# Performance work log

Measured on AMD Instinct MI355X. Metric: run time of the kernel, lower is better.

Reference implementation:

```python
import jax, jax.numpy as jnp
import numpy as np
from jax import lax

SCALES = [4, 8, 16]
K_PER_SCALE = 4


def setup_inputs() -> dict:
    key = jax.random.key(0)
    B, N, D = 32, 4096, 384  # N = 64*64 perfect square
    features = jax.random.normal(key, (B, N, D), dtype=jnp.float32)
    return {"features": features}


def _kmeans_pp(feats, key, k):
    """k-means++ seeding on feats [N, D]; returns [k, D] centers.

    Faithful to torch version: first center uniform random, subsequent
    centers sampled with prob proportional to squared min distance
    (cdist is euclidean; probs = min_dist**2 == squared distance).
    Incremental min over squared distances is equivalent to recomputing
    cdist to all centers and taking the min each iteration.
    """
    N = feats.shape[0]
    k0, k1 = jax.random.split(key)
    idx0 = jax.random.randint(k0, (), 0, N)
    c0 = feats[idx0]  # [D]
    min_sq = jnp.sum((feats - c0) ** 2, axis=1)  # [N] squared dists

    def step(min_sq, kk):
        probs = min_sq / (min_sq.sum() + 1e-8)
        idx = jax.random.categorical(kk, jnp.log(probs + 1e-12))
        c = feats[idx]
        d = jnp.sum((feats - c) ** 2, axis=1)
        return jnp.minimum(min_sq, d), c

    keys = jax.random.split(k1, k - 1)
    _, rest = lax.scan(step, min_sq, keys)  # rest: [k-1, D]
    return jnp.concatenate([c0[None], rest], axis=0)


def reference(features):
    B, N, D = features.shape
    H = W = int(np.sqrt(N))
    x = features.reshape(B, H, W, D)
    base = jax.random.key(42)
    all_slots = []
    for si, s in enumerate(SCALES):
        # adaptive_avg_pool2d with H divisible by s == block mean
        pooled = x.reshape(B, s, H // s, s, W // s, D).mean(axis=(2, 4))  # [B,s,s,D]
        flat = pooled.reshape(B, s * s, D)
        bkeys = jax.random.split(jax.random.fold_in(base, si), B)
        cents = jax.vmap(lambda f, kk: _kmeans_pp(f, kk, K_PER_SCALE))(flat, bkeys)
        all_slots.append(cents)  # [B, k, D]
    return jnp.concatenate(all_slots, axis=1)  # [B, len(scales)*k, D]
```

## Files before the change

kernel.cpp:

```cpp
#include <hip/hip_runtime.h>
#include <stdint.h>

#define D_ 384
#define NPTS 4096
#define W4_OFF 0
#define W8_OFF 196608
#define W16_OFF 983040

__device__ __forceinline__ void tf_round(uint32_t& x0, uint32_t& x1, int r) {
  x0 += x1;
  x1 = (x1 << r) | (x1 >> (32 - r));
  x1 ^= x0;
}

__device__ void tf2x32(uint32_t k0, uint32_t k1, uint32_t x0, uint32_t x1,
                       uint32_t& y0, uint32_t& y1) {
  uint32_t ks2 = k0 ^ k1 ^ 0x1BD11BDAu;
  x0 += k0; x1 += k1;
  tf_round(x0, x1, 13); tf_round(x0, x1, 15); tf_round(x0, x1, 26); tf_round(x0, x1, 6);
  x0 += k1; x1 += ks2 + 1u;
  tf_round(x0, x1, 17); tf_round(x0, x1, 29); tf_round(x0, x1, 16); tf_round(x0, x1, 24);
  x0 += ks2; x1 += k0 + 2u;
  tf_round(x0, x1, 13); tf_round(x0, x1, 15); tf_round(x0, x1, 26); tf_round(x0, x1, 6);
  x0 += k0; x1 += k1 + 3u;
  tf_round(x0, x1, 17); tf_round(x0, x1, 29); tf_round(x0, x1, 16); tf_round(x0, x1, 24);
  x0 += k1; x1 += ks2 + 4u;
  tf_round(x0, x1, 13); tf_round(x0, x1, 15); tf_round(x0, x1, 26); tf_round(x0, x1, 6);
  x0 += ks2; x1 += k0 + 5u;
  y0 = x0; y1 = x1;
}

__global__ __launch_bounds__(256) void pool16_kernel(const float* __restrict__ feats,
                                                     float* __restrict__ ws) {
  int g = blockIdx.x * 256 + threadIdx.x;
  int q = g % 96;
  int cell = (g / 96) & 255;
  int b = g / (96 * 256);
  int ch = cell >> 4, cw = cell & 15;
  const float* fb = feats + (size_t)b * NPTS * D_;
  float ax = 0.f, ay = 0.f, az = 0.f, aw = 0.f;
  #pragma unroll
  for (int dh = 0; dh < 4; ++dh) {
    int h = ch * 4 + dh;
    #pragma unroll
    for (int dw = 0; dw < 4; ++dw) {
      int w = cw * 4 + dw;
      float4 v = *(const float4*)(fb + ((size_t)(h * 64 + w)) * D_ + q * 4);
      ax += v.x; ay += v.y; az += v.z; aw += v.w;
    }
  }
  float4 o = { ax * (1.f/16.f), ay * (1.f/16.f), az * (1.f/16.f), aw * (1.f/16.f) };
  *(float4*)(ws + W16_OFF + ((size_t)(b * 256 + cell)) * D_ + q * 4) = o;
}

__global__ __launch_bounds__(256) void pool8_kernel(float* __restrict__ ws) {
  int g = blockIdx.x * 256 + threadIdx.x;
  int q = g % 96;
  int c8 = (g / 96) & 63;
  int b = g / (96 * 64);
  int p = c8 >> 3, r = c8 & 7;
  float ax = 0.f, ay = 0.f, az = 0.f, aw = 0.f;
  #pragma unroll
  for (int a = 0; a < 2; ++a)
    #pragma unroll
    for (int c = 0; c < 2; ++c) {
      int cell = (p * 2 + a) * 16 + (r * 2 + c);
      float4 v = *(const float4*)(ws + W16_OFF + ((size_t)(b * 256 + cell)) * D_ + q * 4);
      ax += v.x; ay += v.y; az += v.z; aw += v.w;
    }
  float4 o = { ax * 0.25f, ay * 0.25f, az * 0.25f, aw * 0.25f };
  *(float4*)(ws + W8_OFF + ((size_t)(b * 64 + c8)) * D_ + q * 4) = o;
}

__global__ __launch_bounds__(256) void pool4_kernel(float* __restrict__ ws) {
  int g = blockIdx.x * 256 + threadIdx.x;
  int q = g % 96;
  int c4 = (g / 96) & 15;
  int b = g / (96 * 16);
  int p = c4 >> 2, r = c4 & 3;
  float ax = 0.f, ay = 0.f, az = 0.f, aw = 0.f;
  #pragma unroll
  for (int a = 0; a < 2; ++a)
    #pragma unroll
    for (int c = 0; c < 2; ++c) {
      int cell = (p * 2 + a) * 8 + (r * 2 + c);
      float4 v = *(const float4*)(ws + W8_OFF + ((size_t)(b * 64 + cell)) * D_ + q * 4);
      ax += v.x; ay += v.y; az += v.z; aw += v.w;
    }
  float4 o = { ax * 0.25f, ay * 0.25f, az * 0.25f, aw * 0.25f };
  *(float4*)(ws + W4_OFF + ((size_t)(b * 16 + c4)) * D_ + q * 4) = o;
}

__global__ __launch_bounds__(512) void kmeans_kernel(const float* __restrict__ ws,
                                                     float* __restrict__ out) {
  int blk = blockIdx.x;
  int si = blk / 32;
  int b  = blk % 32;
  int n  = (si == 0) ? 16 : (si == 1) ? 64 : 256;

  const float* pooled;
  if (si == 0)      pooled = ws + W4_OFF  + (size_t)b * 16  * D_;
  else if (si == 1) pooled = ws + W8_OFF  + (size_t)b * 64  * D_;
  else              pooled = ws + W16_OFF + (size_t)b * 256 * D_;
  float* ob = out + ((size_t)b * 12 + si * 4) * D_;

  __shared__ __align__(16) float4 csh4[96];
  __shared__ float minsq[256];
  __shared__ uint32_t skey[3][2];
  __shared__ int sidx;
  __shared__ float ssum;
  __shared__ float wred[4];
  __shared__ float wmaxv[4];
  __shared__ int   wmaxi[4];

  int tid  = threadIdx.x;
  int row  = tid >> 1;
  int part = tid & 1;
  int lane = tid & 63;
  int wv   = tid >> 6;

  if (tid == 0) {
    uint32_t f0, f1, bk0, bk1;
    tf2x32(0u, 42u, 0u, (uint32_t)si, f0, f1);
    tf2x32(f0, f1, 0u, (uint32_t)b, bk0, bk1);
    uint32_t k00, k01, k10, k11;
    tf2x32(bk0, bk1, 0u, 0u, k00, k01);
    tf2x32(bk0, bk1, 0u, 1u, k10, k11);
    uint32_t q0, q1, l0, l1;
    tf2x32(k00, k01, 0u, 1u, q0, q1);
    tf2x32(q0, q1, 0u, 0u, l0, l1);
    sidx = (int)((l0 ^ l1) & (uint32_t)(n - 1));
    for (int t = 0; t < 3; ++t) {
      uint32_t a, bb;
      tf2x32(k10, k11, 0u, (uint32_t)t, a, bb);
      skey[t][0] = a; skey[t][1] = bb;
    }
  }
  if (tid < 256) minsq[tid] = 0.f;

  float4 xr[48];
  if (row < n) {
    const float4* rp = (const float4*)(pooled + (size_t)row * D_ + part * 192);
    #pragma unroll
    for (int k = 0; k < 48; ++k) xr[k] = rp[k];
  }
  __syncthreads();

  if (row == sidx) {
    float4* cb = csh4 + part * 48;
    float4* op = (float4*)(ob + part * 192);
    #pragma unroll
    for (int k = 0; k < 48; ++k) { cb[k] = xr[k]; op[k] = xr[k]; }
  }
  __syncthreads();

  if (row < n) {
    float acc = 0.f;
    #pragma unroll
    for (int k = 0; k < 48; ++k) {
      float4 c4 = csh4[part * 48 + k];
      float dx = xr[k].x - c4.x, dy = xr[k].y - c4.y;
      float dz = xr[k].z - c4.z, dw = xr[k].w - c4.w;
      acc += dx * dx; acc += dy * dy; acc += dz * dz; acc += dw * dw;
    }
    acc += __shfl_xor(acc, 1);
    if (part == 0) minsq[row] = acc;
  }
  __syncthreads();

  const float TINY = __uint_as_float(0x00800000u);

  for (int t = 0; t < 3; ++t) {
    if (tid < 256) {
      float v = minsq[tid];
      #pragma unroll
      for (int m = 1; m < 64; m <<= 1) v += __shfl_xor(v, m);
      if (lane == 0) wred[wv] = v;
    }
    __syncthreads();
    if (tid == 0) ssum = ((wred[0] + wred[1]) + (wred[2] + wred[3])) + 1e-8f;
    __syncthreads();

    if (tid < 256) {
      float z = -1e30f;
      if (tid < n) {
        float prob  = minsq[tid] / ssum;
        float logit = logf(prob + 1e-12f);
        uint32_t y0, y1;
        tf2x32(skey[t][0], skey[t][1], 0u, (uint32_t)tid, y0, y1);
        uint32_t bits = y0 ^ y1;
        float f = __uint_as_float((bits >> 9) | 0x3F800000u) - 1.0f;
        float u = (f > 0.f) ? f : TINY;
        z = -logf(-logf(u)) + logit;
      }
      float bv = z; int bi = tid;
      #pragma unroll
      for (int m = 1; m < 64; m <<= 1) {
        float ov = __shfl_xor(bv, m);
        int   oi = __shfl_xor(bi, m);
        if (ov > bv || (ov == bv && oi < bi)) { bv = ov; bi = oi; }
      }
      if (lane == 0) { wmaxv[wv] = bv; wmaxi[wv] = bi; }
    }
    __syncthreads();
    if (tid == 0) {
      float cv = wmaxv[0]; int ci = wmaxi[0];
      for (int w2 = 1; w2 < 4; ++w2)
        if (wmaxv[w2] > cv || (wmaxv[w2] == cv && wmaxi[w2] < ci)) { cv = wmaxv[w2]; ci = wmaxi[w2]; }
      sidx = ci;
    }
    __syncthreads();

    if (row == sidx) {
      float4* cb = csh4 + part * 48;
      float4* op = (float4*)(ob + (size_t)(t + 1) * D_ + part * 192);
      #pragma unroll
      for (int k = 0; k < 48; ++k) { cb[k] = xr[k]; op[k] = xr[k]; }
    }
    __syncthreads();

    if (row < n) {
      float acc = 0.f;
      #pragma unroll
      for (int k = 0; k < 48; ++k) {
        float4 c4 = csh4[part * 48 + k];
        float dx = xr[k].x - c4.x, dy = xr[k].y - c4.y;
        float dz = xr[k].z - c4.z, dw = xr[k].w - c4.w;
        acc += dx * dx; acc += dy * dy; acc += dz * dz; acc += dw * dw;
      }
      acc += __shfl_xor(acc, 1);
      if (part == 0) minsq[row] = fminf(minsq[row], acc);
    }
    __syncthreads();
  }
}

extern "C" void kernel_launch(void* const* d_in, const int* in_sizes, int n_in,
                              void* d_out, int out_size, void* d_ws, size_t ws_size,
                              hipStream_t stream) {
  const float* feats = (const float*)d_in[0];
  float* out = (float*)d_out;
  float* ws  = (float*)d_ws;

  pool16_kernel<<<3072, 256, 0, stream>>>(feats, ws);
  pool8_kernel<<<768, 256, 0, stream>>>(ws);
  pool4_kernel<<<192, 256, 0, stream>>>(ws);
  kmeans_kernel<<<96, 512, 0, stream>>>(ws, out);
}
```

Baseline: 66.43 us.

## Fuse 8x8 and 4x4 pooling into the kmeans kernel from 16x16 pooled data

Drops the separate pool8 and pool4 kernels. The kmeans blocks now compute the coarser pooled rows directly from the 16x16 pooled workspace: the 8-scale rows are averaged in registers, and the 4-scale rows go through a shared-memory buffer. This removes two kernel launches and their workspace round trips. In exchange, the small-scale blocks do extra loads, use more shared memory, and partially unroll the register-load loops.

Result: slower. 127.7 us (+92.2%).

```diff
diff --git a/kernel.cpp b/kernel.cpp
--- a/kernel.cpp
+++ b/kernel.cpp
@@ -3,9 +3,6 @@
 
 #define D_ 384
 #define NPTS 4096
-#define W4_OFF 0
-#define W8_OFF 196608
-#define W16_OFF 983040
 
 __device__ __forceinline__ void tf_round(uint32_t& x0, uint32_t& x1, int r) {
   x0 += x1;
@@ -50,45 +47,7 @@
     }
   }
   float4 o = { ax * (1.f/16.f), ay * (1.f/16.f), az * (1.f/16.f), aw * (1.f/16.f) };
-  *(float4*)(ws + W16_OFF + ((size_t)(b * 256 + cell)) * D_ + q * 4) = o;
-}
-
-__global__ __launch_bounds__(256) void pool8_kernel(float* __restrict__ ws) {
-  int g = blockIdx.x * 256 + threadIdx.x;
-  int q = g % 96;
-  int c8 = (g / 96) & 63;
-  int b = g / (96 * 64);
-  int p = c8 >> 3, r = c8 & 7;
-  float ax = 0.f, ay = 0.f, az = 0.f, aw = 0.f;
-  #pragma unroll
-  for (int a = 0; a < 2; ++a)
-    #pragma unroll
-    for (int c = 0; c < 2; ++c) {
-      int cell = (p * 2 + a) * 16 + (r * 2 + c);
-      float4 v = *(const float4*)(ws + W16_OFF + ((size_t)(b * 256 + cell)) * D_ + q * 4);
-      ax += v.x; ay += v.y; az += v.z; aw += v.w;
-    }
-  float4 o = { ax * 0.25f, ay * 0.25f, az * 0.25f, aw * 0.25f };
-  *(float4*)(ws + W8_OFF + ((size_t)(b * 64 + c8)) * D_ + q * 4) = o;
-}
-
-__global__ __launch_bounds__(256) void pool4_kernel(float* __restrict__ ws) {
-  int g = blockIdx.x * 256 + threadIdx.x;
-  int q = g % 96;
-  int c4 = (g / 96) & 15;
-  int b = g / (96 * 16);
-  int p = c4 >> 2, r = c4 & 3;
-  float ax = 0.f, ay = 0.f, az = 0.f, aw = 0.f;
-  #pragma unroll
-  for (int a = 0; a < 2; ++a)
-    #pragma unroll
-    for (int c = 0; c < 2; ++c) {
-      int cell = (p * 2 + a) * 8 + (r * 2 + c);
-      float4 v = *(const float4*)(ws + W8_OFF + ((size_t)(b * 64 + cell)) * D_ + q * 4);
-      ax += v.x; ay += v.y; az += v.z; aw += v.w;
-    }
-  float4 o = { ax * 0.25f, ay * 0.25f, az * 0.25f, aw * 0.25f };
-  *(float4*)(ws + W4_OFF + ((size_t)(b * 16 + c4)) * D_ + q * 4) = o;
+  *(float4*)(ws + ((size_t)(b * 256 + cell)) * D_ + q * 4) = o;
 }
 
 __global__ __launch_bounds__(512) void kmeans_kernel(const float* __restrict__ ws,
@@ -98,12 +57,10 @@
   int b  = blk % 32;
   int n  = (si == 0) ? 16 : (si == 1) ? 64 : 256;
 
-  const float* pooled;
-  if (si == 0)      pooled = ws + W4_OFF  + (size_t)b * 16  * D_;
-  else if (si == 1) pooled = ws + W8_OFF  + (size_t)b * 64  * D_;
-  else              pooled = ws + W16_OFF + (size_t)b * 256 * D_;
+  const float4* w16b = (const float4*)(ws + (size_t)b * 256 * D_);
   float* ob = out + ((size_t)b * 12 + si * 4) * D_;
 
+  __shared__ __align__(16) float4 p4buf[16 * 96];
   __shared__ __align__(16) float4 csh4[96];
   __shared__ float minsq[256];
   __shared__ uint32_t skey[3][2];
@@ -139,10 +96,61 @@
   if (tid < 256) minsq[tid] = 0.f;
 
   float4 xr[48];
-  if (row < n) {
-    const float4* rp = (const float4*)(pooled + (size_t)row * D_ + part * 192);
-    #pragma unroll
+  if (si == 2) {
+    const float4* rp = w16b + (size_t)row * 96 + part * 48;
+    #pragma unroll 8
     for (int k = 0; k < 48; ++k) xr[k] = rp[k];
+  } else if (si == 1) {
+    if (row < 64) {
+      int p = row >> 3, r = row & 7;
+      int c00 = (p * 2) * 16 + (r * 2);
+      const float4* r00 = w16b + (size_t)c00 * 96 + part * 48;
+      const float4* r01 = w16b + (size_t)(c00 + 1) * 96 + part * 48;
+      const float4* r10 = w16b + (size_t)(c00 + 16) * 96 + part * 48;
+      const float4* r11 = w16b + (size_t)(c00 + 17) * 96 + part * 48;
+      #pragma unroll 4
+      for (int k = 0; k < 48; ++k) {
+        float4 v0 = r00[k], v1 = r01[k], v2 = r10[k], v3 = r11[k];
+        float4 o;
+        o.x = (((v0.x + v1.x) + v2.x) + v3.x) * 0.25f;
+        o.y = (((v0.y + v1.y) + v2.y) + v3.y) * 0.25f;
+        o.z = (((v0.z + v1.z) + v2.z) + v3.z) * 0.25f;
+        o.w = (((v0.w + v1.w) + v2.w) + v3.w) * 0.25f;
+        xr[k] = o;
+      }
+    }
+  } else {
+    int r4 = tid >> 5;
+    int sub = tid & 31;
+    int p = r4 >> 2, r = r4 & 3;
+    for (int it = 0; it < 3; ++it) {
+      int q = sub + it * 32;
+      float ax = 0.f, ay = 0.f, az = 0.f, aw = 0.f;
+      #pragma unroll
+      for (int a = 0; a < 2; ++a)
+        #pragma unroll
+        for (int c = 0; c < 2; ++c) {
+          int p8 = p * 2 + a, r8 = r * 2 + c;
+          float bx = 0.f, by = 0.f, bz = 0.f, bw = 0.f;
+          #pragma unroll
+          for (int a2 = 0; a2 < 2; ++a2)
+            #pragma unroll
+            for (int c2 = 0; c2 < 2; ++c2) {
+              int cell = (p8 * 2 + a2) * 16 + (r8 * 2 + c2);
+              float4 v = w16b[(size_t)cell * 96 + q];
+              bx += v.x; by += v.y; bz += v.z; bw += v.w;
+            }
+          bx *= 0.25f; by *= 0.25f; bz *= 0.25f; bw *= 0.25f;
+          ax += bx; ay += by; az += bz; aw += bw;
+        }
+      float4 o = { ax * 0.25f, ay * 0.25f, az * 0.25f, aw * 0.25f };
+      p4buf[r4 * 96 + q] = o;
+    }
+    __syncthreads();
+    if (row < 16) {
+      #pragma unroll 8
+      for (int k = 0; k < 48; ++k) xr[k] = p4buf[row * 96 + part * 48 + k];
+    }
   }
   __syncthreads();
 
@@ -243,7 +251,5 @@
   float* ws  = (float*)d_ws;
 
   pool16_kernel<<<3072, 256, 0, stream>>>(feats, ws);
-  pool8_kernel<<<768, 256, 0, stream>>>(ws);
-  pool4_kernel<<<192, 256, 0, stream>>>(ws);
   kmeans_kernel<<<96, 512, 0, stream>>>(ws, out);
 }
```
